# Kernel optimization log

Measured on AMD Instinct MI355X. Metric: run time of the kernel, lower is better.

The kernel has to match this reference:

```python
import jax, jax.numpy as jnp
from jax import lax
import numpy as np

PH, PW = 5, 5      # patch_shape; forced to 5x5 by the (batch, F, 27) reshape in AdaptiveConv
F = 32             # adaptive conv output channels
SCALE = 4          # super-resolution upscale factor


def conv2d(x, w, b, padding):
    # x: NCHW, w: OIHW
    y = lax.conv_general_dilated(x, w, (1, 1), padding,
                                 dimension_numbers=('NCHW', 'OIHW', 'NCHW'))
    return y + b[None, :, None, None]


def space_to_batch(x):
    # non-overlapping PHxPW tiles, order (batch, tile_row, tile_col) like the torch loops
    B, C, H, W = x.shape
    hn, wn = H // PH, W // PW
    p = x.reshape(B, C, hn, PH, wn, PW).transpose(0, 2, 4, 1, 3, 5)
    return p.reshape(B * hn * wn, C, PH, PW), (B, hn, wn)


def batch_to_space(p, meta):
    B, hn, wn = meta
    C = p.shape[1]
    out = p.reshape(B, hn, wn, C, PH, PW).transpose(0, 3, 1, 4, 2, 5)
    return out.reshape(B, C, hn * PH, wn * PW)


def unfold3(x):
    # torch F.unfold(x, 3, padding=1): (N, C*9, L) channel-major (c, kh, kw); return (N, L, C*9)
    N, C, H, W = x.shape
    xp = jnp.pad(x, ((0, 0), (0, 0), (1, 1), (1, 1)))
    cols = jnp.stack([xp[:, :, i:i + H, j:j + W]
                      for i in range(3) for j in range(3)], axis=2)  # (N, C, 9, H, W)
    return cols.reshape(N, C * 9, H * W).transpose(0, 2, 1)


def pixel_shuffle(x, r):
    B, Cr2, H, W = x.shape
    C = Cr2 // (r * r)
    return (x.reshape(B, C, r, r, H, W)
             .transpose(0, 1, 4, 2, 5, 3)
             .reshape(B, C, H * r, W * r))


def setup_inputs() -> dict:
    key = jax.random.key(0)
    ks = jax.random.split(key, 13)
    rn = lambda k, shape, s=0.05: jax.random.normal(k, shape, jnp.float32) * s
    return dict(
        x=jax.random.normal(ks[0], (2, 3, 360, 640), jnp.float32),
        w_feat=rn(ks[1], (256, 3, 3, 3)),        b_feat=rn(ks[2], (256,)),
        w_kern=rn(ks[3], (27 * F, 256, 3, 3)),   b_kern=rn(ks[4], (27 * F,)),
        w_badp=rn(ks[5], (F, 256, 3, 3)),        b_badp=rn(ks[6], (F,)),
        w1=rn(ks[7], (128, F, 5, 5)),            b1=rn(ks[8], (128,)),
        w2=rn(ks[9], (32, 128, 3, 3)),           b2=rn(ks[10], (32,)),
        w3=rn(ks[11], (3 * SCALE * SCALE, 32, 3, 3)), b3=rn(ks[12], (3 * SCALE * SCALE,)),
    )


def reference(x, w_feat, b_feat, w_kern, b_kern, w_badp, b_badp,
              w1, b1, w2, b2, w3, b3):
    patches, meta = space_to_batch(x)                        # (N, 3, 5, 5)
    N = patches.shape[0]
    # AdaptiveConv: per-patch dynamic 3x3 conv
    feat = jax.nn.relu(conv2d(patches, w_feat, b_feat, 'VALID'))   # (N, 256, 3, 3)
    kern = conv2d(feat, w_kern, b_kern, 'VALID')                   # (N, 27F, 1, 1)
    kern = kern.reshape(N, F, 27).transpose(0, 2, 1)               # (N, 27, F)
    xu = unfold3(patches)                                          # (N, 25, 27)
    out = jnp.einsum('nlk,nkf->nlf', xu, kern)                     # (N, 25, F)
    out = out.transpose(0, 2, 1).reshape(N, F, PH, PW)
    bias = conv2d(feat, w_badp, b_badp, 'VALID')                   # (N, F, 1, 1)
    out = jax.nn.relu(out + bias)
    sp = batch_to_space(out, meta)                                 # (B, F, H, W)
    # RegularConv stack
    h = jax.nn.relu(conv2d(sp, w1, b1, 'SAME'))
    h = jax.nn.relu(conv2d(h, w2, b2, 'SAME'))
    h = conv2d(h, w3, b3, 'SAME')                                  # (B, 3*r*r, H, W)
    return pixel_shuffle(h, SCALE)                                 # (B, 3, H*r, W*r)
```

## Files before the change

### kernel.cpp

```cpp
#include <hip/hip_runtime.h>
#include <stdint.h>

typedef unsigned short ushort;
typedef __bf16 bf16x8 __attribute__((ext_vector_type(8)));
typedef float f32x4 __attribute__((ext_vector_type(4)));
typedef ushort ushort8 __attribute__((ext_vector_type(8)));
typedef ushort us4 __attribute__((ext_vector_type(4)));

__device__ __forceinline__ float bf2f(ushort u) {
  union { unsigned int i; float f; } v; v.i = ((unsigned int)u) << 16; return v.f;
}
__device__ __forceinline__ ushort f2bf(float f) {
  union { float f; unsigned int i; } v; v.f = f;
  unsigned int r = v.i + 0x7fffu + ((v.i >> 16) & 1u);
  return (ushort)(r >> 16);
}
__device__ __forceinline__ void glds16(const ushort* g, ushort* l) {
  __builtin_amdgcn_global_load_lds(
      (const __attribute__((address_space(1))) void*)g,
      (__attribute__((address_space(3))) void*)l, 16, 0, 0);
}

__global__ __launch_bounds__(256) void pack_kernel(
    const float* __restrict__ w_kern, const float* __restrict__ b_kern,
    const float* __restrict__ w_badp, const float* __restrict__ b_badp,
    ushort* __restrict__ Bt, float* __restrict__ bias896) {
  int idx = blockIdx.x * 256 + threadIdx.x;
  const int total = 896 * 2304;
  if (idx < total) {
    int o = idx / 2304, k = idx - o * 2304;
    int c = k & 255, pos = k >> 8;
    float v = (o < 864) ? w_kern[(o * 256 + c) * 9 + pos]
                        : w_badp[((o - 864) * 256 + c) * 9 + pos];
    Bt[idx] = f2bf(v);
  } else if (idx < total + 896) {
    int o = idx - total;
    bias896[o] = (o < 864) ? b_kern[o] : b_badp[o - 864];
  }
}

__global__ __launch_bounds__(256) void pack2_kernel(
    const float* __restrict__ w1, const float* __restrict__ w2,
    const float* __restrict__ w3, ushort* __restrict__ wp1,
    ushort* __restrict__ wp2, ushort* __restrict__ wp3) {
  int idx = blockIdx.x * 256 + threadIdx.x;
  if (idx < 102400) {
    int t = idx >> 12, rm = idx & 4095, o = rm >> 5, c = rm & 31;
    wp1[idx] = f2bf(w1[(o * 32 + c) * 25 + t]);
  } else if (idx < 102400 + 36864) {
    int j = idx - 102400;
    int t = j >> 12, rm = j & 4095, o = rm >> 7, c = rm & 127;
    wp2[j] = f2bf(w2[(o * 128 + c) * 9 + t]);
  } else if (idx < 102400 + 36864 + 13824) {
    int j = idx - 139264;
    int t = j / 1536, rm = j - t * 1536, o = rm >> 5, c = rm & 31;
    wp3[j] = f2bf(w3[(o * 32 + c) * 9 + t]);
  }
}

__global__ __launch_bounds__(256) void feat_kernel(
    const float* __restrict__ x, const float* __restrict__ w_feat,
    const float* __restrict__ b_feat, ushort* __restrict__ feat) {
  __shared__ float xp[4][3][5][5];
  const int t = threadIdx.x;
  const int n0 = blockIdx.x * 4;
  for (int e = t; e < 300; e += 256) {
    int p = e / 75, rem = e - p * 75;
    int ci = rem / 25, r = rem - ci * 25, i = r / 5, j = r - i * 5;
    int n = n0 + p;
    int b = n / 9216, ph = (n >> 7) % 72, pw = n & 127;
    xp[p][ci][i][j] = x[((b * 3 + ci) * 360 + ph * 5 + i) * 640 + pw * 5 + j];
  }
  float wf[27];
#pragma unroll
  for (int m = 0; m < 27; ++m) wf[m] = w_feat[t * 27 + m];
  const float bv = b_feat[t];
  __syncthreads();
  for (int p = 0; p < 4; ++p) {
    ushort* dst = feat + (size_t)(n0 + p) * 2304 + t;
#pragma unroll
    for (int pi = 0; pi < 3; ++pi)
#pragma unroll
      for (int pj = 0; pj < 3; ++pj) {
        float acc = bv;
#pragma unroll
        for (int ci = 0; ci < 3; ++ci)
#pragma unroll
          for (int ki = 0; ki < 3; ++ki)
#pragma unroll
            for (int kj = 0; kj < 3; ++kj)
              acc = fmaf(xp[p][ci][pi + ki][pj + kj], wf[ci * 9 + ki * 3 + kj], acc);
        dst[(pi * 3 + pj) * 256] = f2bf(fmaxf(acc, 0.f));
      }
  }
}

__global__ __launch_bounds__(256) void gemm_kernel(
    const ushort* __restrict__ A, const ushort* __restrict__ Bt,
    const float* __restrict__ bias, ushort* __restrict__ C) {
  const int K = 2304, N = 896;
  __shared__ __align__(16) ushort lA[128 * 32];
  __shared__ __align__(16) ushort lB[128 * 32];
  const int bid = blockIdx.x;
  const int xcd = bid & 7, j = bid >> 3;
  const int mblk = xcd * 18 + j / 7, nblk = j % 7;
  const int m0 = mblk * 128, n0 = nblk * 128;
  const int t = threadIdx.x;
  const int lane = t & 63, wave = t >> 6;
  const int wm = wave >> 1, wn = wave & 1;
  f32x4 acc[4][4] = {};
  const ushort* gA = A + (size_t)(m0 + (t >> 2)) * K + (t & 3) * 8;
  const ushort* gB = Bt + (size_t)(n0 + (t >> 2)) * K + (t & 3) * 8;
  ushort* dA0 = &lA[wave * 512];
  ushort* dA1 = &lA[2048 + wave * 512];
  ushort* dB0 = &lB[wave * 512];
  ushort* dB1 = &lB[2048 + wave * 512];
  const int aoff = (wm * 64 + (lane & 15)) * 32 + (lane >> 4) * 8;
  const int boff = (wn * 64 + (lane & 15)) * 32 + (lane >> 4) * 8;
  for (int kt = 0; kt < K; kt += 32) {
    __syncthreads();
    glds16(gA + kt, dA0);
    glds16(gA + 64 * K + kt, dA1);
    glds16(gB + kt, dB0);
    glds16(gB + 64 * K + kt, dB1);
    __syncthreads();
    bf16x8 af[4], bfr[4];
#pragma unroll
    for (int mi = 0; mi < 4; ++mi) {
      ushort8 tmp = *(const ushort8*)(&lA[aoff + mi * 512]);
      af[mi] = __builtin_bit_cast(bf16x8, tmp);
    }
#pragma unroll
    for (int ni = 0; ni < 4; ++ni) {
      ushort8 tmp = *(const ushort8*)(&lB[boff + ni * 512]);
      bfr[ni] = __builtin_bit_cast(bf16x8, tmp);
    }
#pragma unroll
    for (int mi = 0; mi < 4; ++mi)
#pragma unroll
      for (int ni = 0; ni < 4; ++ni)
        acc[mi][ni] = __builtin_amdgcn_mfma_f32_16x16x32_bf16(af[mi], bfr[ni], acc[mi][ni], 0, 0, 0);
  }
#pragma unroll
  for (int ni = 0; ni < 4; ++ni) {
    int col = n0 + wn * 64 + ni * 16 + (lane & 15);
    float bv = bias[col];
#pragma unroll
    for (int mi = 0; mi < 4; ++mi) {
      int row0 = m0 + wm * 64 + mi * 16 + (lane >> 4) * 4;
#pragma unroll
      for (int r = 0; r < 4; ++r)
        C[(size_t)(row0 + r) * N + col] = f2bf(acc[mi][ni][r] + bv);
    }
  }
}

__global__ __launch_bounds__(256) void apply_kernel(
    const float* __restrict__ x, const ushort* __restrict__ kernbias,
    ushort* __restrict__ sp) {
  __shared__ float xp[8][3][7][7];
  __shared__ ushort outl[8][32][25];
  const int t = threadIdx.x;
  const int n0 = blockIdx.x * 8;
  const int b = n0 / 9216, ph = (n0 >> 7) % 72, pw0 = n0 & 127;
  for (int e = t; e < 8 * 3 * 49; e += 256) ((float*)xp)[e] = 0.f;
  __syncthreads();
  for (int e = t; e < 600; e += 256) {
    int p = e / 75, rem = e - p * 75;
    int ci = rem / 25, r = rem - ci * 25, i = r / 5, j = r - i * 5;
    xp[p][ci][i + 1][j + 1] = x[((b * 3 + ci) * 360 + ph * 5 + i) * 640 + (pw0 + p) * 5 + j];
  }
  __syncthreads();
  const int p = t >> 5, f = t & 31;
  const int n = n0 + p;
  float kk[27];
#pragma unroll
  for (int k = 0; k < 27; ++k) kk[k] = bf2f(kernbias[(size_t)n * 896 + f * 27 + k]);
  const float bv = bf2f(kernbias[(size_t)n * 896 + 864 + f]);
  for (int l = 0; l < 25; ++l) {
    int li = l / 5, lj = l - li * 5;
    float s = bv;
#pragma unroll
    for (int k = 0; k < 27; ++k) {
      int ci = k / 9, rm = k - ci * 9, ki = rm / 3, kj = rm - ki * 3;
      s = fmaf(xp[p][ci][li + ki][lj + kj], kk[k], s);
    }
    outl[p][f][l] = f2bf(fmaxf(s, 0.f));
  }
  __syncthreads();
  for (int e = t; e < 6400; e += 256) {
    int f2 = e & 31;
    int idx = e >> 5;
    int i = idx / 40, c40 = idx - i * 40;
    int pp = c40 / 5, j = c40 - pp * 5;
    sp[(((size_t)b * 360 + ph * 5 + i) * 640 + pw0 * 5 + c40) * 32 + f2] = outl[pp][f2][i * 5 + j];
  }
}

__global__ __launch_bounds__(512, 4) void conv1_kernel(
    const ushort* __restrict__ sp, const ushort* __restrict__ wp1,
    const float* __restrict__ b1, ushort* __restrict__ h1) {
  __shared__ ushort8 lin[8 * 4 * 69];
  __shared__ ushort8 wbuf[2][1024];
  const int t = threadIdx.x;
  const int lane = t & 63, wave = t >> 6;
  const int wh = wave >> 1, wn = wave & 1;
  const int lp = lane & 15, lk = lane >> 4;
  const int w0 = blockIdx.x * 64, h0 = blockIdx.y * 4, b = blockIdx.z;
  for (int u = t; u < 8 * 4 * 68; u += 512) {
    int c8 = u & 3, rest = u >> 2;
    int wx = rest % 68, r = rest / 68;
    int gh = h0 - 2 + r, gw = w0 - 2 + wx;
    ushort8 v = {};
    if ((unsigned)gh < 360u && (unsigned)gw < 640u)
      v = *(const ushort8*)(sp + (((size_t)b * 360 + gh) * 640 + gw) * 32 + c8 * 8);
    lin[(r * 4 + c8) * 69 + wx] = v;
  }
  ushort* wd0 = (ushort*)&wbuf[0][wave * 64];
  ushort* wd1 = (ushort*)&wbuf[1][wave * 64];
  glds16(wp1 + t * 8, wd0);
  __syncthreads();

  f32x4 acc[4][4] = {};
#pragma unroll
  for (int tp = 0; tp < 25; ++tp) {
    if (tp < 24)
      glds16(wp1 + (tp + 1) * 4096 + t * 8, ((tp + 1) & 1) ? wd1 : wd0);
    const int ki = tp / 5, kj = tp % 5;
    const ushort8* wb8 = wbuf[tp & 1];
    bf16x8 W[4], Af[4];
#pragma unroll
    for (int nf = 0; nf < 4; ++nf)
      W[nf] = __builtin_bit_cast(bf16x8, wb8[(wn * 64 + nf * 16 + lp) * 4 + lk]);
    const int ab = (wh + ki) * 276 + lk * 69 + lp + kj;
#pragma unroll
    for (int mf = 0; mf < 4; ++mf)
      Af[mf] = __builtin_bit_cast(bf16x8, lin[ab + mf * 16]);
#pragma unroll
    for (int mf = 0; mf < 4; ++mf)
#pragma unroll
      for (int nf = 0; nf < 4; ++nf)
        acc[mf][nf] = __builtin_amdgcn_mfma_f32_16x16x32_bf16(W[nf], Af[mf], acc[mf][nf], 0, 0, 0);
    if (tp < 24) __syncthreads();
  }

  const int h = h0 + wh;
#pragma unroll
  for (int nf = 0; nf < 4; ++nf) {
    const int oc0 = wn * 64 + nf * 16 + lk * 4;
    f32x4 bv = *(const f32x4*)(b1 + oc0);
#pragma unroll
    for (int mf = 0; mf < 4; ++mf) {
      const int w = w0 + mf * 16 + lp;
      us4 pk;
#pragma unroll
      for (int r = 0; r < 4; ++r) pk[r] = f2bf(fmaxf(acc[mf][nf][r] + bv[r], 0.f));
      *(us4*)(&h1[(((size_t)b * 360 + h) * 640 + w) * 128 + oc0]) = pk;
    }
  }
}

__device__ __forceinline__ void c2_load(ushort8* stg, const ushort* __restrict__ h1,
                                        int t, int b, int h0, int w0, int cb) {
#pragma unroll
  for (int j = 0; j < 7; ++j) {
    int u = t + j * 256;
    ushort8 v = {};
    if (u < 1584) {
      int r = u / 264, rem = u - r * 264;
      int c8 = rem / 66, wx = rem - c8 * 66;
      int gh = h0 - 1 + r, gw = w0 - 1 + wx;
      if ((unsigned)gh < 360u && (unsigned)gw < 640u)
        v = *(const ushort8*)(h1 + (((size_t)b * 360 + gh) * 640 + gw) * 128 + cb * 32 + c8 * 8);
    }
    stg[j] = v;
  }
}
__device__ __forceinline__ void c2_write(const ushort8* stg, ushort8* buf, int t) {
#pragma unroll
  for (int j = 0; j < 7; ++j) {
    int u = t + j * 256;
    if (u < 1584) {
      int r = u / 264, rem = u - r * 264;
      int c8 = rem / 66, wx = rem - c8 * 66;
      buf[c8 * 414 + r * 69 + wx] = stg[j];
    }
  }
}
__device__ __forceinline__ void c2_compute(const ushort8* buf, const ushort* __restrict__ wp2,
                                           int cb, int wave, int lp, int lk, f32x4 acc[4][2]) {
#pragma unroll
  for (int ki = 0; ki < 3; ++ki) {
    const int rb = lk * 414 + (wave + ki) * 69;
#pragma unroll
    for (int kj = 0; kj < 3; ++kj) {
      const int tap = ki * 3 + kj;
      bf16x8 bfr[2];
#pragma unroll
      for (int nf = 0; nf < 2; ++nf) {
        ushort8 tmp = *(const ushort8*)(wp2 + tap * 4096 + nf * 2048 + lp * 128 + cb * 32 + lk * 8);
        bfr[nf] = __builtin_bit_cast(bf16x8, tmp);
      }
      bf16x8 afr[4];
#pragma unroll
      for (int mf = 0; mf < 4; ++mf)
        afr[mf] = __builtin_bit_cast(bf16x8, buf[rb + lp + mf * 16 + kj]);
#pragma unroll
      for (int mf = 0; mf < 4; ++mf)
#pragma unroll
        for (int nf = 0; nf < 2; ++nf)
          acc[mf][nf] = __builtin_amdgcn_mfma_f32_16x16x32_bf16(bfr[nf], afr[mf], acc[mf][nf], 0, 0, 0);
    }
  }
}

__global__ __launch_bounds__(256) void conv2_kernel(
    const ushort* __restrict__ h1, const ushort* __restrict__ wp2,
    const float* __restrict__ b2, ushort* __restrict__ h2) {
  __shared__ ushort8 lin[2][4 * 414];
  const int t = threadIdx.x;
  const int lane = t & 63, wave = t >> 6;
  const int lp = lane & 15, lk = lane >> 4;
  const int w0 = blockIdx.x * 64, h0 = blockIdx.y * 4, b = blockIdx.z;
  f32x4 acc[4][2] = {};
  ushort8 stg[7];
  c2_load(stg, h1, t, b, h0, w0, 0);
#pragma unroll
  for (int it = 0; it < 5; ++it) {
    __syncthreads();
    if (it < 4) c2_write(stg, lin[it & 1], t);
    if (it < 3) c2_load(stg, h1, t, b, h0, w0, it + 1);
    if (it >= 1) c2_compute(lin[(it - 1) & 1], wp2, it - 1, wave, lp, lk, acc);
  }
  const int h = h0 + wave;
#pragma unroll
  for (int nf = 0; nf < 2; ++nf) {
    const int oc0 = nf * 16 + lk * 4;
    f32x4 bv = *(const f32x4*)(b2 + oc0);
#pragma unroll
    for (int mf = 0; mf < 4; ++mf) {
      const int w = w0 + mf * 16 + lp;
      us4 pk;
#pragma unroll
      for (int r = 0; r < 4; ++r) pk[r] = f2bf(fmaxf(acc[mf][nf][r] + bv[r], 0.f));
      *(us4*)(&h2[(((size_t)b * 360 + h) * 640 + w) * 32 + oc0]) = pk;
    }
  }
}

__global__ __launch_bounds__(256) void conv3_kernel(
    const ushort* __restrict__ h2, const ushort* __restrict__ wp3,
    const float* __restrict__ b3, float* __restrict__ out) {
  __shared__ ushort8 lin[4 * 4 * 67];
  const int t = threadIdx.x;
  const int lane = t & 63, wave = t >> 6;
  const int wh = wave & 1, wm = wave >> 1;
  const int lp = lane & 15, lk = lane >> 4;
  const int w0 = blockIdx.x * 64, h0 = blockIdx.y * 2, b = blockIdx.z;
  for (int u = t; u < 4 * 4 * 66; u += 256) {
    int c8 = u & 3, rest = u >> 2;
    int wx = rest % 66, r = rest / 66;
    int gh = h0 - 1 + r, gw = w0 - 1 + wx;
    ushort8 v = {};
    if (gh >= 0 && gh < 360 && gw >= 0 && gw < 640)
      v = *(const ushort8*)(h2 + (((size_t)b * 360 + gh) * 640 + gw) * 32 + c8 * 8);
    lin[(r * 4 + c8) * 67 + wx] = v;
  }
  __syncthreads();
  f32x4 acc[2][3] = {};
  const int abase = lk * 67 + wm * 32 + lp;
  const ushort* wbase = wp3 + lp * 32 + lk * 8;
#pragma unroll
  for (int ki = 0; ki < 3; ++ki) {
#pragma unroll
    for (int kj = 0; kj < 3; ++kj) {
      const int tap = ki * 3 + kj;
      bf16x8 bfr[3];
#pragma unroll
      for (int nf = 0; nf < 3; ++nf) {
        ushort8 tmp = *(const ushort8*)(wbase + (size_t)tap * 1536 + nf * 512);
        bfr[nf] = __builtin_bit_cast(bf16x8, tmp);
      }
      bf16x8 afr[2];
#pragma unroll
      for (int mf = 0; mf < 2; ++mf)
        afr[mf] = __builtin_bit_cast(bf16x8, lin[(wh + ki) * 268 + abase + mf * 16 + kj]);
#pragma unroll
      for (int mf = 0; mf < 2; ++mf)
#pragma unroll
        for (int nf = 0; nf < 3; ++nf)
          acc[mf][nf] = __builtin_amdgcn_mfma_f32_16x16x32_bf16(bfr[nf], afr[mf], acc[mf][nf], 0, 0, 0);
    }
  }
  const int h = h0 + wh;
#pragma unroll
  for (int nf = 0; nf < 3; ++nf) {
    f32x4 bv = *(const f32x4*)(b3 + nf * 16 + lk * 4);
#pragma unroll
    for (int mf = 0; mf < 2; ++mf) {
      const int w = w0 + wm * 32 + mf * 16 + lp;
      f32x4 o;
#pragma unroll
      for (int r = 0; r < 4; ++r) o[r] = acc[mf][nf][r] + bv[r];
      *(f32x4*)(&out[(((size_t)b * 3 + nf) * 1440 + h * 4 + lk) * 2560 + (size_t)w * 4]) = o;
    }
  }
}

extern "C" void kernel_launch(void* const* d_in, const int* in_sizes, int n_in,
                              void* d_out, int out_size, void* d_ws, size_t ws_size,
                              hipStream_t stream) {
  const float* x      = (const float*)d_in[0];
  const float* w_feat = (const float*)d_in[1];
  const float* b_feat = (const float*)d_in[2];
  const float* w_kern = (const float*)d_in[3];
  const float* b_kern = (const float*)d_in[4];
  const float* w_badp = (const float*)d_in[5];
  const float* b_badp = (const float*)d_in[6];
  const float* w1 = (const float*)d_in[7];
  const float* b1 = (const float*)d_in[8];
  const float* w2 = (const float*)d_in[9];
  const float* b2 = (const float*)d_in[10];
  const float* w3 = (const float*)d_in[11];
  const float* b3 = (const float*)d_in[12];

  char* ws = (char*)d_ws;
  ushort* feat     = (ushort*)(ws);
  ushort* h1       = (ushort*)(ws);
  ushort* kernbias = (ushort*)(ws + 117964800);
  ushort* h2       = (ushort*)(ws + 117964800);
  ushort* wp1      = (ushort*)(ws + 147456000);
  ushort* wp2      = (ushort*)(ws + 147660800);
  ushort* wp3      = (ushort*)(ws + 147734528);
  ushort* sp       = (ushort*)(ws + 150994944);
  ushort* Bt       = (ushort*)(ws + 180486144);
  float*  bias896  = (float*)(ws + 184614912);

  pack_kernel<<<(896 * 2304 + 896 + 255) / 256, 256, 0, stream>>>(
      w_kern, b_kern, w_badp, b_badp, Bt, bias896);
  feat_kernel<<<4608, 256, 0, stream>>>(x, w_feat, b_feat, feat);
  gemm_kernel<<<1008, 256, 0, stream>>>(feat, Bt, bias896, kernbias);
  apply_kernel<<<2304, 256, 0, stream>>>(x, kernbias, sp);
  pack2_kernel<<<598, 256, 0, stream>>>(w1, w2, w3, wp1, wp2, wp3);
  conv1_kernel<<<dim3(10, 90, 2), 512, 0, stream>>>(sp, wp1, b1, h1);
  conv2_kernel<<<dim3(10, 90, 2), 256, 0, stream>>>(h1, wp2, b2, h2);
  conv3_kernel<<<dim3(10, 180, 2), 256, 0, stream>>>(h2, wp3, b3, (float*)d_out);
}
```

Baseline: 469.6 us.

## Double-buffer GEMM LDS tiles and XOR-swizzle layout to avoid bank conflicts

```diff
diff --git a/kernel.cpp b/kernel.cpp
--- a/kernel.cpp
+++ b/kernel.cpp
@@ -99,8 +99,8 @@
     const ushort* __restrict__ A, const ushort* __restrict__ Bt,
     const float* __restrict__ bias, ushort* __restrict__ C) {
   const int K = 2304, N = 896;
-  __shared__ __align__(16) ushort lA[128 * 32];
-  __shared__ __align__(16) ushort lB[128 * 32];
+  __shared__ __align__(16) ushort lA[2][128 * 32];
+  __shared__ __align__(16) ushort lB[2][128 * 32];
   const int bid = blockIdx.x;
   const int xcd = bid & 7, j = bid >> 3;
   const int mblk = xcd * 18 + j / 7, nblk = j % 7;
@@ -108,46 +108,60 @@
   const int t = threadIdx.x;
   const int lane = t & 63, wave = t >> 6;
   const int wm = wave >> 1, wn = wave & 1;
+  const int lp = lane & 15, lk = lane >> 4;
   f32x4 acc[4][4] = {};
-  const ushort* gA = A + (size_t)(m0 + (t >> 2)) * K + (t & 3) * 8;
-  const ushort* gB = Bt + (size_t)(n0 + (t >> 2)) * K + (t & 3) * 8;
-  ushort* dA0 = &lA[wave * 512];
-  ushort* dA1 = &lA[2048 + wave * 512];
-  ushort* dB0 = &lB[wave * 512];
-  ushort* dB1 = &lB[2048 + wave * 512];
-  const int aoff = (wm * 64 + (lane & 15)) * 32 + (lane >> 4) * 8;
-  const int boff = (wn * 64 + (lane & 15)) * 32 + (lane >> 4) * 8;
-  for (int kt = 0; kt < K; kt += 32) {
+  const int srow = t >> 2;
+  const int sslot = (t & 3) ^ ((srow >> 1) & 3);
+  const ushort* gA = A + (size_t)(m0 + srow) * K + sslot * 8;
+  const ushort* gB = Bt + (size_t)(n0 + srow) * K + sslot * 8;
+  const int swz = lk ^ ((lp >> 1) & 3);
+  const int aoff = (wm * 64 + lp) * 32 + swz * 8;
+  const int boff = (wn * 64 + lp) * 32 + swz * 8;
+
+#define GSTAGE(buf, kt)                                   \
+  do {                                                    \
+    glds16(gA + (kt), &lA[buf][wave * 512]);              \
+    glds16(gA + 64 * K + (kt), &lA[buf][2048 + wave * 512]); \
+    glds16(gB + (kt), &lB[buf][wave * 512]);              \
+    glds16(gB + 64 * K + (kt), &lB[buf][2048 + wave * 512]); \
+  } while (0)
+
+#define GCOMP(buf)                                                            \
+  do {                                                                        \
+    bf16x8 af[4], bfr[4];                                                     \
+    _Pragma("unroll") for (int mi = 0; mi < 4; ++mi)                          \
+        af[mi] = __builtin_bit_cast(bf16x8,                                   \
+            *(const ushort8*)(&lA[buf][aoff + mi * 512]));                    \
+    _Pragma("unroll") for (int ni = 0; ni < 4; ++ni)                          \
+        bfr[ni] = __builtin_bit_cast(bf16x8,                                  \
+            *(const ushort8*)(&lB[buf][boff + ni * 512]));                    \
+    _Pragma("unroll") for (int mi = 0; mi < 4; ++mi)                          \
+        _Pragma("unroll") for (int ni = 0; ni < 4; ++ni)                      \
+            acc[mi][ni] = __builtin_amdgcn_mfma_f32_16x16x32_bf16(            \
+                af[mi], bfr[ni], acc[mi][ni], 0, 0, 0);                       \
+  } while (0)
+
+  GSTAGE(0, 0);
+  __syncthreads();
+#pragma unroll 1
+  for (int kt = 0; kt < K; kt += 64) {
+    GSTAGE(1, kt + 32);
+    GCOMP(0);
     __syncthreads();
-    glds16(gA + kt, dA0);
-    glds16(gA + 64 * K + kt, dA1);
-    glds16(gB + kt, dB0);
-    glds16(gB + 64 * K + kt, dB1);
+    if (kt + 64 < K) GSTAGE(0, kt + 64);
+    GCOMP(1);
     __syncthreads();
-    bf16x8 af[4], bfr[4];
+  }
+#undef GSTAGE
+#undef GCOMP
+
+#pragma unroll
+  for (int ni = 0; ni < 4; ++ni) {
+    int col = n0 + wn * 64 + ni * 16 + lp;
+    float bv = bias[col];
 #pragma unroll
     for (int mi = 0; mi < 4; ++mi) {
-      ushort8 tmp = *(const ushort8*)(&lA[aoff + mi * 512]);
-      af[mi] = __builtin_bit_cast(bf16x8, tmp);
-    }
-#pragma unroll
-    for (int ni = 0; ni < 4; ++ni) {
-      ushort8 tmp = *(const ushort8*)(&lB[boff + ni * 512]);
-      bfr[ni] = __builtin_bit_cast(bf16x8, tmp);
-    }
-#pragma unroll
-    for (int mi = 0; mi < 4; ++mi)
-#pragma unroll
-      for (int ni = 0; ni < 4; ++ni)
-        acc[mi][ni] = __builtin_amdgcn_mfma_f32_16x16x32_bf16(af[mi], bfr[ni], acc[mi][ni], 0, 0, 0);
-  }
-#pragma unroll
-  for (int ni = 0; ni < 4; ++ni) {
-    int col = n0 + wn * 64 + ni * 16 + (lane & 15);
-    float bv = bias[col];
-#pragma unroll
-    for (int mi = 0; mi < 4; ++mi) {
-      int row0 = m0 + wm * 64 + mi * 16 + (lane >> 4) * 4;
+      int row0 = m0 + wm * 64 + mi * 16 + lk * 4;
 #pragma unroll
       for (int r = 0; r < 4; ++r)
         C[(size_t)(row0 + r) * N + col] = f2bf(acc[mi][ni][r] + bv);
```

New measurement: 466.2 us. Within noise of the previous version (-0.7%).
